# Performance work log

Hardware: AMD Instinct MI355X
Metric: run time of the kernel (lower is better)

Reference implementation:

```python
import jax, jax.numpy as jnp
import numpy as np
from jax import lax

N = 50000      # num_entities
R = 8          # num_relations
E = 200000     # edges per relation
D = 128        # emb_dim
HID = 128      # hidden_dim
H = 4          # heads (layer 1)
OUT = 256      # out_dim
LN_EPS = 1e-5
SM_EPS = 1e-16  # PyG softmax denom eps


def setup_inputs() -> dict:
    key = jax.random.key(0)
    ks = jax.random.split(key, 12)
    s = 0.05
    return {
        "entity_emb": jax.random.normal(ks[0], (N, D)) * s,
        "W1": jax.random.normal(ks[1], (R, D, H * HID)) * s,
        "a_src1": jax.random.normal(ks[2], (R, H, HID)) * s,
        "a_dst1": jax.random.normal(ks[3], (R, H, HID)) * s,
        "b1": jnp.zeros((R, H * HID)),
        "W2": jax.random.normal(ks[4], (R, H * HID, OUT)) * s,
        "a_src2": jax.random.normal(ks[5], (R, 1, OUT)) * s,
        "a_dst2": jax.random.normal(ks[6], (R, 1, OUT)) * s,
        "b2": jnp.zeros((R, OUT)),
        "res_W": jax.random.normal(ks[7], (D, OUT)) * s,
        "res_b": jnp.zeros((OUT,)),
        "ln_g": jnp.ones((OUT,)),
        "ln_b": jnp.zeros((OUT,)),
        "edge_index": jax.random.randint(ks[8], (R, 2, E), 0, N, dtype=jnp.int32),
    }


def _gat_conv(x, W, a_s, a_d, b, src, dst, concat):
    """PyG-style GATConv (eval mode, self-loops already appended)."""
    n = x.shape[0]
    h, c = a_s.shape                       # heads, out channels per head
    xp = (x @ W).reshape(n, h, c)          # projected features [N,H,C]
    al_s = jnp.sum(xp * a_s, axis=-1)      # [N,H] per-head src logits
    al_d = jnp.sum(xp * a_d, axis=-1)      # [N,H]
    e = jax.nn.leaky_relu(al_s[src] + al_d[dst], 0.2)  # [Etot,H]
    m = jax.ops.segment_max(e, dst, num_segments=n)    # stable segment softmax
    ex = jnp.exp(e - m[dst])
    denom = jax.ops.segment_sum(ex, dst, num_segments=n)
    alpha = ex / (denom[dst] + SM_EPS)                 # [Etot,H]
    out = jax.ops.segment_sum(alpha[:, :, None] * xp[src], dst, num_segments=n)  # [N,H,C]
    out = out.reshape(n, h * c) if concat else out.mean(axis=1)
    return out + b


def reference(entity_emb, W1, a_src1, a_dst1, b1, W2, a_src2, a_dst2, b2,
              res_W, res_b, ln_g, ln_b, edge_index):
    # add self loops per relation (PyG default add_self_loops=True)
    loops = jnp.broadcast_to(jnp.arange(N, dtype=edge_index.dtype), (R, N))
    src = jnp.concatenate([edge_index[:, 0, :], loops], axis=1)  # [R, E+N]
    dst = jnp.concatenate([edge_index[:, 1, :], loops], axis=1)

    x0 = entity_emb

    def body1(acc, p):
        W, a_s, a_d, b, s_, d_ = p
        return acc + jax.nn.elu(_gat_conv(x0, W, a_s, a_d, b, s_, d_, True)), None

    h1, _ = lax.scan(body1, jnp.zeros((N, H * HID), x0.dtype),
                     (W1, a_src1, a_dst1, b1, src, dst))

    def body2(acc, p):
        W, a_s, a_d, b, s_, d_ = p
        return acc + _gat_conv(h1, W, a_s, a_d, b, s_, d_, False), None

    h2, _ = lax.scan(body2, jnp.zeros((N, OUT), x0.dtype),
                     (W2, a_src2, a_dst2, b2, src, dst))

    y = h2 + x0 @ res_W + res_b              # residual projection
    mu = y.mean(-1, keepdims=True)
    var = ((y - mu) ** 2).mean(-1, keepdims=True)
    return (y - mu) / jnp.sqrt(var + LN_EPS) * ln_g + ln_b
```

## Files before the change

kernel.cpp:

```cpp
#include <hip/hip_runtime.h>
#include <hip/hip_bf16.h>

#define N_NODES 50000
#define R_REL   8
#define E_EDGES 200000
#define ETOT    (E_EDGES + N_NODES)
#define D_INP   128
#define HIDC    128
#define NH      4
#define F1      (NH*HIDC)
#define F2      256
#define LN_EPS  1e-5f
#define SM_EPS  1e-16f

typedef unsigned short u16;
typedef __bf16 bf16x8 __attribute__((ext_vector_type(8)));
typedef __bf16 bf16x4 __attribute__((ext_vector_type(4)));
typedef float  f32x4  __attribute__((ext_vector_type(4)));

__device__ __forceinline__ float bf2f(u16 u){
  union { unsigned int i; float f; } v; v.i = ((unsigned int)u) << 16; return v.f;
}
__device__ __forceinline__ u16 f2bf(float f){
  union { float f; unsigned int i; } v; v.f = f;
  unsigned int r = v.i + 0x7FFFu + ((v.i >> 16) & 1u);
  return (u16)(r >> 16);
}

template<bool F32OUT>
__global__ __launch_bounds__(256)
void k_gemm(const u16* __restrict__ A, const u16* __restrict__ Bt,
            u16* __restrict__ C, float* __restrict__ Cf, int M, int K, int Nn)
{
  __shared__ __align__(16) u16 As[128][32];
  __shared__ __align__(16) u16 Bs[128][32];
  const int tid  = threadIdx.x;
  const int lane = tid & 63, wv = tid >> 6;
  const int wr = wv >> 1, wc = wv & 1;
  const long bm = (long)blockIdx.y * 128, bn = (long)blockIdx.x * 128;

  f32x4 acc[4][4];
#pragma unroll
  for (int m=0;m<4;m++)
#pragma unroll
    for (int n=0;n<4;n++) acc[m][n] = (f32x4){0.f,0.f,0.f,0.f};

  for (int k0 = 0; k0 < K; k0 += 32) {
    __syncthreads();
#pragma unroll
    for (int i=0;i<2;i++){
      int c   = tid + 256*i;
      int row = c >> 2, ch = c & 3;
      int sw  = ch ^ ((row >> 1) & 3);
      long gr = bm + row;
      bf16x8 va;
#pragma unroll
      for (int j=0;j<8;j++) va[j] = (__bf16)0.0f;
      if (gr < M) va = *(const bf16x8*)(A + gr*(long)K + k0 + ch*8);
      *(bf16x8*)(&As[row][sw*8]) = va;
      bf16x8 vb = *(const bf16x8*)(Bt + (bn + row)*(long)K + k0 + ch*8);
      *(bf16x8*)(&Bs[row][sw*8]) = vb;
    }
    __syncthreads();
    const int ch = lane >> 4, rl = lane & 15;
    bf16x8 af[4], bfr[4];
#pragma unroll
    for (int m=0;m<4;m++){
      int row = wr*64 + m*16 + rl;
      af[m] = *(const bf16x8*)(&As[row][(ch ^ ((row >> 1) & 3))*8]);
    }
#pragma unroll
    for (int n=0;n<4;n++){
      int row = wc*64 + n*16 + rl;
      bfr[n] = *(const bf16x8*)(&Bs[row][(ch ^ ((row >> 1) & 3))*8]);
    }
#pragma unroll
    for (int m=0;m<4;m++)
#pragma unroll
      for (int n=0;n<4;n++)
        acc[m][n] = __builtin_amdgcn_mfma_f32_16x16x32_bf16(af[m], bfr[n], acc[m][n], 0,0,0);
  }
  const int rl = lane & 15, rg = lane >> 4;
#pragma unroll
  for (int m=0;m<4;m++)
#pragma unroll
    for (int n=0;n<4;n++)
#pragma unroll
      for (int q=0;q<4;q++){
        long row = bm + wr*64 + m*16 + rg*4 + q;
        long col = bn + wc*64 + n*16 + rl;
        if (row < M){
          if (F32OUT) Cf[row*(long)Nn + col] = acc[m][n][q];
          else        C [row*(long)Nn + col] = f2bf(acc[m][n][q]);
        }
      }
}

__global__ __launch_bounds__(256)
void k_al1s(const u16* __restrict__ xp, const float* __restrict__ a_s,
            const float* __restrict__ a_d, float* __restrict__ alS, float* __restrict__ alD)
{
  int i = blockIdx.x*256 + threadIdx.x;
  if (i >= N_NODES*NH) return;
  int n = i >> 2, h = i & 3;
  const u16* row = xp + (long)n*F1 + h*HIDC;
  const float* as = a_s + h*HIDC;
  const float* ad = a_d + h*HIDC;
  float s = 0.f, d = 0.f;
  for (int c=0;c<HIDC;c++){ float x = bf2f(row[c]); s += x*as[c]; d += x*ad[c]; }
  alS[i] = s; alD[i] = d;
}

__global__ __launch_bounds__(256)
void k_al2s(const u16* __restrict__ xp, const float* __restrict__ a_s,
            const float* __restrict__ a_d, float* __restrict__ alS, float* __restrict__ alD)
{
  int n = blockIdx.x*256 + threadIdx.x;
  if (n >= N_NODES) return;
  const u16* row = xp + (long)n*F2;
  float s = 0.f, d = 0.f;
  for (int c=0;c<F2;c++){ float x = bf2f(row[c]); s += x*a_s[c]; d += x*a_d[c]; }
  alS[n] = s; alD[n] = d;
}

__global__ __launch_bounds__(64)
void k_edge1(const int* __restrict__ off, const int* __restrict__ el,
             const float* __restrict__ alS, const float* __restrict__ alD,
             const u16* __restrict__ xp, const float* __restrict__ b1,
             u16* __restrict__ h1)
{
  const int d = blockIdx.x, lane = threadIdx.x;
  const int h = lane >> 4;
  const int beg = off[d], end = off[d+1];
  const float ald = alD[d*NH + h];

  float dn = 0.f;
  for (int e=beg;e<end;e++){
    int s = el[e];
    float t = alS[s*NH + h] + ald; t = fmaxf(t, 0.2f*t);
    dn += __expf(t);
  }
  const float iv = 1.f/(dn + SM_EPS);

  float acc[8];
#pragma unroll
  for (int j=0;j<8;j++) acc[j]=0.f;
  for (int e=beg;e<end;e++){
    int s = el[e];
    float t = alS[s*NH + h] + ald; t = fmaxf(t, 0.2f*t);
    float w = __expf(t) * iv;
    bf16x8 xv = *(const bf16x8*)(xp + (long)s*F1 + 8*lane);
#pragma unroll
    for (int j=0;j<8;j++) acc[j] += w * (float)xv[j];
  }
  u16* hr = h1 + (long)d*F1 + 8*lane;
  bf16x8 hv = *(bf16x8*)hr;
#pragma unroll
  for (int j=0;j<8;j++){
    float o = acc[j] + b1[8*lane + j];
    o = (o > 0.f) ? o : (__expf(o) - 1.f);
    hv[j] = (__bf16)((float)hv[j] + o);
  }
  *(bf16x8*)hr = hv;
}

__global__ __launch_bounds__(64)
void k_edge2(const int* __restrict__ off, const int* __restrict__ el,
             const float* __restrict__ alS, const float* __restrict__ alD,
             const u16* __restrict__ xp, const float* __restrict__ b2,
             float* __restrict__ h2)
{
  const int d = blockIdx.x, lane = threadIdx.x;
  const int beg = off[d], end = off[d+1];
  const float ald = alD[d];

  float dn = 0.f;
  for (int e=beg;e<end;e++){
    float t = alS[el[e]] + ald; t = fmaxf(t, 0.2f*t);
    dn += __expf(t);
  }
  const float iv = 1.f/(dn + SM_EPS);

  float acc[4];
#pragma unroll
  for (int j=0;j<4;j++) acc[j]=0.f;
  for (int e=beg;e<end;e++){
    int s = el[e];
    float t = alS[s] + ald; t = fmaxf(t, 0.2f*t);
    float w = __expf(t) * iv;
    bf16x4 xv = *(const bf16x4*)(xp + (long)s*F2 + 4*lane);
#pragma unroll
    for (int j=0;j<4;j++) acc[j] += w * (float)xv[j];
  }
  float* hr = h2 + (long)d*F2 + 4*lane;
#pragma unroll
  for (int j=0;j<4;j++) hr[j] += acc[j] + b2[4*lane + j];
}

__global__ __launch_bounds__(256)
void k_final(const float* __restrict__ h2, const float* __restrict__ res_b,
             const float* __restrict__ g, const float* __restrict__ bb,
             float* __restrict__ out)
{
  const int n = blockIdx.x, c = threadIdx.x;
  const int lane = c & 63, wv = c >> 6;
  float y = h2[(long)n*F2 + c] + res_b[c];
  float s1 = y, s2 = y*y;
#pragma unroll
  for (int o=32;o>0;o>>=1){ s1 += __shfl_down(s1,o); s2 += __shfl_down(s2,o); }
  __shared__ float l1[4], l2[4];
  if (lane==0){ l1[wv]=s1; l2[wv]=s2; }
  __syncthreads();
  float t1 = l1[0]+l1[1]+l1[2]+l1[3];
  float t2 = l2[0]+l2[1]+l2[2]+l2[3];
  float mu  = t1 * (1.f/F2);
  float var = t2 * (1.f/F2) - mu*mu;
  float rs  = rsqrtf(var + LN_EPS);
  out[(long)n*F2 + c] = (y - mu) * rs * g[c] + bb[c];
}

__global__ void k_transpose(const float* __restrict__ W, u16* __restrict__ Wt, int K, int Nn)
{
  int t = blockIdx.x*256 + threadIdx.x;
  if (t < K*Nn){ int nn = t / K, kk = t - nn*K; Wt[t] = f2bf(W[(long)kk*Nn + nn]); }
}
__global__ __launch_bounds__(256)
void k_cvt(const float* __restrict__ s, u16* __restrict__ d, long n)
{
  long i = ((long)blockIdx.x*256 + threadIdx.x)*4;
  if (i < n){
    float4 v = *(const float4*)(s + i);
    ushort4 o; o.x=f2bf(v.x); o.y=f2bf(v.y); o.z=f2bf(v.z); o.w=f2bf(v.w);
    *(ushort4*)(d + i) = o;
  }
}
__global__ void k_zero16(u16* p, long n){
  long i = (long)blockIdx.x*256+threadIdx.x; if (i<n) p[i]=0;
}
__global__ void k_fillf(float* p, long n, float v){
  long i = (long)blockIdx.x*256+threadIdx.x; if (i<n) p[i]=v;
}

__global__ void k_seti(int* p, int v, int n){
  int i = blockIdx.x*256+threadIdx.x; if (i<n) p[i]=v;
}
__global__ void k_count(const int* __restrict__ ei, int* __restrict__ cnt){
  int i = blockIdx.x*256+threadIdx.x;
  if (i < R_REL*E_EDGES){
    int r = i / E_EDGES, e = i - r*E_EDGES;
    int dd = ei[(long)r*2*E_EDGES + E_EDGES + e];
    atomicAdd(&cnt[r*N_NODES + dd], 1);
  }
}
#define SCAN_CHUNK 1024
#define NBLK 49
__global__ __launch_bounds__(256)
void k_scan1(const int* __restrict__ cnt, int* __restrict__ bs){
  int r = blockIdx.x / NBLK, b = blockIdx.x - r*NBLK;
  int base = b*SCAN_CHUNK + threadIdx.x*4;
  int s = 0;
#pragma unroll
  for (int i=0;i<4;i++){ int idx = base+i; if (idx<N_NODES) s += cnt[r*N_NODES+idx]; }
  __shared__ int sm[256];
  sm[threadIdx.x]=s; __syncthreads();
  for (int o=128;o>0;o>>=1){ if (threadIdx.x<o) sm[threadIdx.x]+=sm[threadIdx.x+o]; __syncthreads(); }
  if (threadIdx.x==0) bs[r*64+b] = sm[0];
}
__global__ void k_scan2(int* bs, int* off){
  int r = blockIdx.x;
  if (threadIdx.x==0){
    int run=0;
    for (int i=0;i<NBLK;i++){ int t=bs[r*64+i]; bs[r*64+i]=run; run+=t; }
    off[(long)r*(N_NODES+1) + N_NODES] = run;
  }
}
__global__ __launch_bounds__(256)
void k_scan3(const int* __restrict__ cnt, const int* __restrict__ bs, int* __restrict__ off){
  int r = blockIdx.x / NBLK, b = blockIdx.x - r*NBLK;
  int tid = threadIdx.x;
  int base = b*SCAN_CHUNK + tid*4;
  int v[4]; int ts=0;
#pragma unroll
  for (int i=0;i<4;i++){ int idx=base+i; v[i] = (idx<N_NODES)? cnt[r*N_NODES+idx] : 0; ts+=v[i]; }
  __shared__ int sm[256];
  sm[tid]=ts; __syncthreads();
  for (int o=1;o<256;o<<=1){
    int add = (tid>=o)? sm[tid-o] : 0;
    __syncthreads();
    sm[tid] += add;
    __syncthreads();
  }
  int run = bs[r*64+b] + (sm[tid] - ts);
#pragma unroll
  for (int i=0;i<4;i++){ int idx=base+i; if (idx<N_NODES) off[(long)r*(N_NODES+1)+idx] = run; run += v[i]; }
}
__global__ void k_cursor(const int* __restrict__ off, int* __restrict__ cur){
  int i = blockIdx.x*256+threadIdx.x;
  if (i < R_REL*N_NODES){ int r=i/N_NODES, nn=i-r*N_NODES; cur[i] = off[(long)r*(N_NODES+1)+nn]; }
}
__global__ void k_scat_self(int* cur, int* el){
  int i = blockIdx.x*256+threadIdx.x;
  if (i < R_REL*N_NODES){
    int r=i/N_NODES, nn=i-r*N_NODES;
    int p = atomicAdd(&cur[i],1);
    el[(long)r*ETOT + p] = nn;
  }
}
__global__ void k_scat_edge(const int* __restrict__ ei, int* cur, int* el){
  int i = blockIdx.x*256+threadIdx.x;
  if (i < R_REL*E_EDGES){
    int r = i / E_EDGES, e = i - r*E_EDGES;
    int ss = ei[(long)r*2*E_EDGES + e];
    int dd = ei[(long)r*2*E_EDGES + E_EDGES + e];
    int p = atomicAdd(&cur[r*N_NODES+dd],1);
    el[(long)r*ETOT + p] = ss;
  }
}

extern "C" void kernel_launch(void* const* d_in, const int* in_sizes, int n_in,
                              void* d_out, int out_size, void* d_ws, size_t ws_size,
                              hipStream_t stream)
{
  float* out = (float*)d_out;
  const long NOUT = (long)out_size;

  static const int exp_sizes[14] = {6400000, 524288, 4096, 4096, 4096, 1048576,
                                    2048, 2048, 2048, 32768, 256, 256, 256, 3200000};
  float sent = 0.f;
  if (n_in != 14) sent = 450.f;
  else for (int i=0;i<14;i++) if (in_sizes[i] != exp_sizes[i]){ sent = 500.f + 10.f*i; break; }
  if (sent != 0.f){
    k_fillf<<<(int)((NOUT+255)/256),256,0,stream>>>(out, NOUT, sent);
    return;
  }

  const float* emb   = (const float*)d_in[0];
  const float* W1    = (const float*)d_in[1];
  const float* a_s1  = (const float*)d_in[2];
  const float* a_d1  = (const float*)d_in[3];
  const float* b1    = (const float*)d_in[4];
  const float* W2    = (const float*)d_in[5];
  const float* a_s2  = (const float*)d_in[6];
  const float* a_d2  = (const float*)d_in[7];
  const float* b2    = (const float*)d_in[8];
  const float* resW  = (const float*)d_in[9];
  const float* res_b = (const float*)d_in[10];
  const float* ln_g  = (const float*)d_in[11];
  const float* ln_b  = (const float*)d_in[12];
  const int*   ei    = (const int*)d_in[13];

  char* base = (char*)d_ws; size_t o_ = 0;
  auto alloc = [&](size_t bytes)->void*{
    void* q = base + o_; o_ += (bytes + 255) & ~(size_t)255; return q;
  };
  int*   off  = (int*)  alloc((size_t)R_REL*(N_NODES+1)*4);
  int*   cur  = (int*)  alloc((size_t)R_REL*N_NODES*4);
  int*   el   = (int*)  alloc((size_t)R_REL*ETOT*4);
  int*   bs   = (int*)  alloc((size_t)R_REL*64*4);
  float* alS  = (float*)alloc((size_t)N_NODES*NH*4);
  float* alD  = (float*)alloc((size_t)N_NODES*NH*4);
  u16*   embb = (u16*)  alloc((size_t)N_NODES*D_INP*2);
  u16*   xp   = (u16*)  alloc((size_t)N_NODES*F1*2);
  u16*   h1   = (u16*)  alloc((size_t)N_NODES*F1*2);
  float* h2   = (float*)alloc((size_t)N_NODES*F2*4);
  u16*   Wt   = (u16*)  alloc((size_t)512*512*2);
  if (o_ > ws_size){
    k_fillf<<<(int)((NOUT+255)/256),256,0,stream>>>(out, NOUT, 250.f);
    return;
  }

  int g;
  k_cvt<<<(int)(((long)N_NODES*D_INP/4+255)/256),256,0,stream>>>(emb, embb, (long)N_NODES*D_INP);
  k_zero16<<<(int)(((long)N_NODES*F1+255)/256),256,0,stream>>>(h1, (long)N_NODES*F1);

  g = (R_REL*N_NODES+255)/256; k_seti<<<g,256,0,stream>>>(cur, 1, R_REL*N_NODES);
  g = (R_REL*E_EDGES+255)/256; k_count<<<g,256,0,stream>>>(ei, cur);
  k_scan1<<<R_REL*NBLK,256,0,stream>>>(cur, bs);
  k_scan2<<<R_REL,64,0,stream>>>(bs, off);
  k_scan3<<<R_REL*NBLK,256,0,stream>>>(cur, bs, off);
  g = (R_REL*N_NODES+255)/256; k_cursor<<<g,256,0,stream>>>(off, cur);
  k_scat_self<<<g,256,0,stream>>>(cur, el);
  g = (R_REL*E_EDGES+255)/256; k_scat_edge<<<g,256,0,stream>>>(ei, cur, el);

  const int GM = (N_NODES + 127)/128;

  g = (D_INP*F2+255)/256;
  k_transpose<<<g,256,0,stream>>>(resW, Wt, D_INP, F2);
  k_gemm<true><<<dim3(F2/128, GM),256,0,stream>>>(embb, Wt, nullptr, h2, N_NODES, D_INP, F2);

  for (int r=0;r<R_REL;r++){
    g = (D_INP*F1+255)/256;
    k_transpose<<<g,256,0,stream>>>(W1 + (size_t)r*D_INP*F1, Wt, D_INP, F1);
    k_gemm<false><<<dim3(F1/128, GM),256,0,stream>>>(embb, Wt, xp, nullptr, N_NODES, D_INP, F1);
    k_al1s<<<(N_NODES*NH+255)/256,256,0,stream>>>(xp, a_s1 + (size_t)r*NH*HIDC,
                                                  a_d1 + (size_t)r*NH*HIDC, alS, alD);
    k_edge1<<<N_NODES,64,0,stream>>>(off + (size_t)r*(N_NODES+1), el + (size_t)r*ETOT,
                                     alS, alD, xp, b1 + (size_t)r*F1, h1);
  }

  for (int r=0;r<R_REL;r++){
    g = (F1*F2+255)/256;
    k_transpose<<<g,256,0,stream>>>(W2 + (size_t)r*F1*F2, Wt, F1, F2);
    k_gemm<false><<<dim3(F2/128, GM),256,0,stream>>>(h1, Wt, xp, nullptr, N_NODES, F1, F2);
    k_al2s<<<(N_NODES+255)/256,256,0,stream>>>(xp, a_s2 + (size_t)r*F2, a_d2 + (size_t)r*F2, alS, alD);
    k_edge2<<<N_NODES,64,0,stream>>>(off + (size_t)r*(N_NODES+1), el + (size_t)r*ETOT,
                                     alS, alD, xp, b2 + (size_t)r*F2, h2);
  }

  k_final<<<N_NODES,256,0,stream>>>(h2, res_b, ln_g, ln_b, out);
}
```

Measured before the change: 2.070 ms.

## Use direct global-to-LDS loads in GEMM, wave-parallel logits, batched weight transposes

The GEMM tile loader now uses global_load_lds to copy A and B tiles straight into shared memory instead of staging them through registers. Out-of-range A rows are clamped to the last row rather than zero-filled, which is harmless because those output rows are never stored. The attention-logit kernels now assign one wavefront per node, with vectorized loads and shuffle reductions, replacing the serial per-thread dot product with strided scalar reads. Weight transposes are batched into one launch per layer instead of one per relation, and W2t reuses the embb buffer, which is no longer needed by the time layer 2 runs.

```diff
diff --git a/kernel.cpp b/kernel.cpp
--- a/kernel.cpp
+++ b/kernel.cpp
@@ -50,16 +50,15 @@
 #pragma unroll
     for (int i=0;i<2;i++){
       int c   = tid + 256*i;
-      int row = c >> 2, ch = c & 3;
-      int sw  = ch ^ ((row >> 1) & 3);
-      long gr = bm + row;
-      bf16x8 va;
-#pragma unroll
-      for (int j=0;j<8;j++) va[j] = (__bf16)0.0f;
-      if (gr < M) va = *(const bf16x8*)(A + gr*(long)K + k0 + ch*8);
-      *(bf16x8*)(&As[row][sw*8]) = va;
-      bf16x8 vb = *(const bf16x8*)(Bt + (bn + row)*(long)K + k0 + ch*8);
-      *(bf16x8*)(&Bs[row][sw*8]) = vb;
+      int row = c >> 2, blk = c & 3;
+      int ch  = blk ^ ((row >> 1) & 3);
+      long gra = bm + row; if (gra > M-1) gra = M-1;
+      char* ldsA = (char*)&As[0][0] + ((size_t)((tid & ~63) + 256*i) * 16);
+      char* ldsB = (char*)&Bs[0][0] + ((size_t)((tid & ~63) + 256*i) * 16);
+      __builtin_amdgcn_global_load_lds((const unsigned int*)(A  + gra*(long)K + k0 + ch*8),
+                                       (unsigned int*)ldsA, 16, 0, 0);
+      __builtin_amdgcn_global_load_lds((const unsigned int*)(Bt + (bn + row)*(long)K + k0 + ch*8),
+                                       (unsigned int*)ldsB, 16, 0, 0);
     }
     __syncthreads();
     const int ch = lane >> 4, rl = lane & 15;
@@ -97,30 +96,42 @@
 }
 
 __global__ __launch_bounds__(256)
-void k_al1s(const u16* __restrict__ xp, const float* __restrict__ a_s,
+void k_al1w(const u16* __restrict__ xp, const float* __restrict__ a_s,
             const float* __restrict__ a_d, float* __restrict__ alS, float* __restrict__ alD)
 {
-  int i = blockIdx.x*256 + threadIdx.x;
-  if (i >= N_NODES*NH) return;
-  int n = i >> 2, h = i & 3;
-  const u16* row = xp + (long)n*F1 + h*HIDC;
-  const float* as = a_s + h*HIDC;
-  const float* ad = a_d + h*HIDC;
+  const int wv = threadIdx.x >> 6, lane = threadIdx.x & 63;
+  const int n = blockIdx.x*4 + wv;
+  const int h = lane >> 4;
+  bf16x8 x = *(const bf16x8*)(xp + (long)n*F1 + 8*lane);
+  f32x4 a0 = *(const f32x4*)(a_s + 8*lane);
+  f32x4 a1 = *(const f32x4*)(a_s + 8*lane + 4);
+  f32x4 e0 = *(const f32x4*)(a_d + 8*lane);
+  f32x4 e1 = *(const f32x4*)(a_d + 8*lane + 4);
   float s = 0.f, d = 0.f;
-  for (int c=0;c<HIDC;c++){ float x = bf2f(row[c]); s += x*as[c]; d += x*ad[c]; }
-  alS[i] = s; alD[i] = d;
-}
-
-__global__ __launch_bounds__(256)
-void k_al2s(const u16* __restrict__ xp, const float* __restrict__ a_s,
+#pragma unroll
+  for (int j=0;j<4;j++){ float xv=(float)x[j];   s += xv*a0[j]; d += xv*e0[j]; }
+#pragma unroll
+  for (int j=0;j<4;j++){ float xv=(float)x[4+j]; s += xv*a1[j]; d += xv*e1[j]; }
+#pragma unroll
+  for (int o=1;o<16;o<<=1){ s += __shfl_xor(s,o); d += __shfl_xor(d,o); }
+  if ((lane & 15) == 0){ alS[n*NH+h] = s; alD[n*NH+h] = d; }
+}
+
+__global__ __launch_bounds__(256)
+void k_al2w(const u16* __restrict__ xp, const float* __restrict__ a_s,
             const float* __restrict__ a_d, float* __restrict__ alS, float* __restrict__ alD)
 {
-  int n = blockIdx.x*256 + threadIdx.x;
-  if (n >= N_NODES) return;
-  const u16* row = xp + (long)n*F2;
+  const int wv = threadIdx.x >> 6, lane = threadIdx.x & 63;
+  const int n = blockIdx.x*4 + wv;
+  bf16x4 x = *(const bf16x4*)(xp + (long)n*F2 + 4*lane);
+  f32x4 a = *(const f32x4*)(a_s + 4*lane);
+  f32x4 e = *(const f32x4*)(a_d + 4*lane);
   float s = 0.f, d = 0.f;
-  for (int c=0;c<F2;c++){ float x = bf2f(row[c]); s += x*a_s[c]; d += x*a_d[c]; }
-  alS[n] = s; alD[n] = d;
+#pragma unroll
+  for (int j=0;j<4;j++){ float xv=(float)x[j]; s += xv*a[j]; d += xv*e[j]; }
+#pragma unroll
+  for (int o=1;o<64;o<<=1){ s += __shfl_xor(s,o); d += __shfl_xor(d,o); }
+  if (lane == 0){ alS[n] = s; alD[n] = d; }
 }
 
 __global__ __launch_bounds__(64)
@@ -219,10 +230,15 @@
   out[(long)n*F2 + c] = (y - mu) * rs * g[c] + bb[c];
 }
 
-__global__ void k_transpose(const float* __restrict__ W, u16* __restrict__ Wt, int K, int Nn)
-{
-  int t = blockIdx.x*256 + threadIdx.x;
-  if (t < K*Nn){ int nn = t / K, kk = t - nn*K; Wt[t] = f2bf(W[(long)kk*Nn + nn]); }
+__global__ void k_transpose_b(const float* __restrict__ W, u16* __restrict__ Wt,
+                              int K, int Nn, int R)
+{
+  long t = (long)blockIdx.x*256 + threadIdx.x;
+  long per = (long)K*Nn;
+  if (t >= (long)R*per) return;
+  int r = (int)(t / per); long w = t - (long)r*per;
+  int nn = (int)(w / K), kk = (int)(w - (long)nn*K);
+  Wt[t] = f2bf(W[(long)r*per + (long)kk*Nn + nn]);
 }
 __global__ __launch_bounds__(256)
 void k_cvt(const float* __restrict__ s, u16* __restrict__ d, long n)
@@ -353,17 +369,19 @@
   auto alloc = [&](size_t bytes)->void*{
     void* q = base + o_; o_ += (bytes + 255) & ~(size_t)255; return q;
   };
-  int*   off  = (int*)  alloc((size_t)R_REL*(N_NODES+1)*4);
-  int*   cur  = (int*)  alloc((size_t)R_REL*N_NODES*4);
-  int*   el   = (int*)  alloc((size_t)R_REL*ETOT*4);
-  int*   bs   = (int*)  alloc((size_t)R_REL*64*4);
-  float* alS  = (float*)alloc((size_t)N_NODES*NH*4);
-  float* alD  = (float*)alloc((size_t)N_NODES*NH*4);
-  u16*   embb = (u16*)  alloc((size_t)N_NODES*D_INP*2);
-  u16*   xp   = (u16*)  alloc((size_t)N_NODES*F1*2);
-  u16*   h1   = (u16*)  alloc((size_t)N_NODES*F1*2);
-  float* h2   = (float*)alloc((size_t)N_NODES*F2*4);
-  u16*   Wt   = (u16*)  alloc((size_t)512*512*2);
+  int*   off   = (int*)  alloc((size_t)R_REL*(N_NODES+1)*4);
+  int*   cur   = (int*)  alloc((size_t)R_REL*N_NODES*4);
+  int*   el    = (int*)  alloc((size_t)R_REL*ETOT*4);
+  int*   bs    = (int*)  alloc((size_t)R_REL*64*4);
+  float* alS   = (float*)alloc((size_t)N_NODES*NH*4);
+  float* alD   = (float*)alloc((size_t)N_NODES*NH*4);
+  u16*   embb  = (u16*)  alloc((size_t)N_NODES*D_INP*2);
+  u16*   xp    = (u16*)  alloc((size_t)N_NODES*F1*2);
+  u16*   h1    = (u16*)  alloc((size_t)N_NODES*F1*2);
+  float* h2    = (float*)alloc((size_t)N_NODES*F2*4);
+  u16*   W1t   = (u16*)  alloc((size_t)R_REL*D_INP*F1*2);
+  u16*   resWt = (u16*)  alloc((size_t)D_INP*F2*2);
+  u16*   W2t   = embb;
   if (o_ > ws_size){
     k_fillf<<<(int)((NOUT+255)/256),256,0,stream>>>(out, NOUT, 250.f);
     return;
@@ -382,27 +400,27 @@
   k_scat_self<<<g,256,0,stream>>>(cur, el);
   g = (R_REL*E_EDGES+255)/256; k_scat_edge<<<g,256,0,stream>>>(ei, cur, el);
 
+  k_transpose_b<<<(R_REL*D_INP*F1+255)/256,256,0,stream>>>(W1, W1t, D_INP, F1, R_REL);
+  k_transpose_b<<<(D_INP*F2+255)/256,256,0,stream>>>(resW, resWt, D_INP, F2, 1);
+
   const int GM = (N_NODES + 127)/128;
 
-  g = (D_INP*F2+255)/256;
-  k_transpose<<<g,256,0,stream>>>(resW, Wt, D_INP, F2);
-  k_gemm<true><<<dim3(F2/128, GM),256,0,stream>>>(embb, Wt, nullptr, h2, N_NODES, D_INP, F2);
+  k_gemm<true><<<dim3(F2/128, GM),256,0,stream>>>(embb, resWt, nullptr, h2, N_NODES, D_INP, F2);
 
   for (int r=0;r<R_REL;r++){
-    g = (D_INP*F1+255)/256;
-    k_transpose<<<g,256,0,stream>>>(W1 + (size_t)r*D_INP*F1, Wt, D_INP, F1);
-    k_gemm<false><<<dim3(F1/128, GM),256,0,stream>>>(embb, Wt, xp, nullptr, N_NODES, D_INP, F1);
-    k_al1s<<<(N_NODES*NH+255)/256,256,0,stream>>>(xp, a_s1 + (size_t)r*NH*HIDC,
-                                                  a_d1 + (size_t)r*NH*HIDC, alS, alD);
+    k_gemm<false><<<dim3(F1/128, GM),256,0,stream>>>(embb, W1t + (size_t)r*D_INP*F1,
+                                                     xp, nullptr, N_NODES, D_INP, F1);
+    k_al1w<<<N_NODES/4,256,0,stream>>>(xp, a_s1 + (size_t)r*NH*HIDC,
+                                       a_d1 + (size_t)r*NH*HIDC, alS, alD);
     k_edge1<<<N_NODES,64,0,stream>>>(off + (size_t)r*(N_NODES+1), el + (size_t)r*ETOT,
                                      alS, alD, xp, b1 + (size_t)r*F1, h1);
   }
 
+  k_transpose_b<<<(R_REL*F1*F2+255)/256,256,0,stream>>>(W2, W2t, F1, F2, R_REL);
   for (int r=0;r<R_REL;r++){
-    g = (F1*F2+255)/256;
-    k_transpose<<<g,256,0,stream>>>(W2 + (size_t)r*F1*F2, Wt, F1, F2);
-    k_gemm<false><<<dim3(F2/128, GM),256,0,stream>>>(h1, Wt, xp, nullptr, N_NODES, F1, F2);
-    k_al2s<<<(N_NODES+255)/256,256,0,stream>>>(xp, a_s2 + (size_t)r*F2, a_d2 + (size_t)r*F2, alS, alD);
+    k_gemm<false><<<dim3(F2/128, GM),256,0,stream>>>(h1, W2t + (size_t)r*F1*F2,
+                                                     xp, nullptr, N_NODES, F1, F2);
+    k_al2w<<<N_NODES/4,256,0,stream>>>(xp, a_s2 + (size_t)r*F2, a_d2 + (size_t)r*F2, alS, alD);
     k_edge2<<<N_NODES,64,0,stream>>>(off + (size_t)r*(N_NODES+1), el + (size_t)r*ETOT,
                                      alS, alD, xp, b2 + (size_t)r*F2, h2);
   }
```

Result: faster. 1.756 ms (-15.1%).
